# Kernel tuning notes

Hardware: AMD Instinct MI355X
Metric: run time of the kernel (lower is better)

The kernel has to match this reference:

```python
import jax, jax.numpy as jnp
import numpy as np

B, S, E, H = 2, 2048, 1024, 16
HD = E // H
CLAMP = 5.0


def setup_inputs() -> dict:
    key = jax.random.key(0)
    k1, k2, k3, k4 = jax.random.split(key, 4)
    # xavier-uniform-ish scale for weights
    lim_qkv = float(np.sqrt(6.0 / (E + 3 * E)))
    lim_o = float(np.sqrt(6.0 / (E + E)))
    return {
        "x": jax.random.normal(k1, (B, S, E), dtype=jnp.float32),
        "attn_bias": jax.random.normal(k2, (B, H, S, S), dtype=jnp.float32),
        "Wqkv": jax.random.uniform(k3, (3 * E, E), dtype=jnp.float32, minval=-lim_qkv, maxval=lim_qkv),
        "bqkv": jnp.zeros((3 * E,), dtype=jnp.float32),
        "Wo": jax.random.uniform(k4, (E, E), dtype=jnp.float32, minval=-lim_o, maxval=lim_o),
        "bo": jnp.zeros((E,), dtype=jnp.float32),
    }


def reference(x, attn_bias, Wqkv, bqkv, Wo, bo):
    b, s, e = x.shape
    # QKV projection: [B,S,3E] -> [B,S,H,3*HD] -> [B,H,S,3*HD]
    qkv = jnp.einsum("bse,fe->bsf", x, Wqkv) + bqkv
    qkv = qkv.reshape(b, s, H, 3 * HD).transpose(0, 2, 1, 3)
    q, k, v = jnp.split(qkv, 3, axis=-1)  # each [B,H,S,HD]
    # logits: bias added BEFORE 1/sqrt(d_k) scaling (as in source)
    logits = jnp.einsum("bhqd,bhkd->bhqk", q, k)
    logits = (logits + attn_bias) / jnp.sqrt(jnp.float32(HD))
    logits = jnp.clip(logits, -CLAMP, CLAMP)
    attn = jax.nn.softmax(logits, axis=-1)
    vals = jnp.einsum("bhqk,bhkd->bhqd", attn, v)
    vals = vals.transpose(0, 2, 1, 3).reshape(b, s, e)
    return jnp.einsum("bse,fe->bsf", vals, Wo) + bo
```

## Files before the change

### kernel.cpp

```cpp
#include <hip/hip_runtime.h>
#include <hip/hip_bf16.h>

#define NB 2
#define NS 2048
#define NE 1024
#define NH 16
#define HD 64

typedef __hip_bfloat16 bf16;
typedef __attribute__((ext_vector_type(8))) short bf16x8;
typedef __attribute__((ext_vector_type(4))) float f32x4;

typedef __attribute__((address_space(3))) void* lds_p;
typedef const __attribute__((address_space(1))) void* glb_p;

#define MFMA16(a, b, c) __builtin_amdgcn_mfma_f32_16x16x32_bf16((a), (b), (c), 0, 0, 0)

__device__ __forceinline__ void gl_lds16(const void* g, void* l) {
    __builtin_amdgcn_global_load_lds((glb_p)g, (lds_p)l, 16, 0, 0);
}

__device__ __forceinline__ bf16x8 ldv8(const bf16* p) { return *(const bf16x8*)p; }

__global__ __launch_bounds__(256) void cast3_k(const float* __restrict__ x,
                                               const float* __restrict__ wqkv,
                                               const float* __restrict__ wo,
                                               bf16* __restrict__ xb,
                                               bf16* __restrict__ wqkvb,
                                               bf16* __restrict__ wob) {
    const int n_x = NB * NS * NE / 4;
    const int n_q = 3 * NE * NE / 4;
    const int n_o = NE * NE / 4;
    int i = blockIdx.x * 256 + threadIdx.x;
    const float* in;
    bf16* out;
    int j;
    if (i < n_x) {
        in = x; out = xb; j = i;
    } else if (i < n_x + n_q) {
        in = wqkv; out = wqkvb; j = i - n_x;
    } else if (i < n_x + n_q + n_o) {
        in = wo; out = wob; j = i - n_x - n_q;
    } else {
        return;
    }
    float4 v = ((const float4*)in)[j];
    union { ushort4 u; bf16 b[4]; } pk;
    pk.b[0] = __float2bfloat16(v.x);
    pk.b[1] = __float2bfloat16(v.y);
    pk.b[2] = __float2bfloat16(v.z);
    pk.b[3] = __float2bfloat16(v.w);
    ((ushort4*)out)[j] = pk.u;
}

__global__ __launch_bounds__(256) void qkv_gemm(const bf16* __restrict__ A,
                                                const bf16* __restrict__ Bm,
                                                const float* __restrict__ bqkv,
                                                bf16* __restrict__ Qb, bf16* __restrict__ Kb,
                                                bf16* __restrict__ Vtb) {
    __shared__ bf16 As[128 * 32];
    __shared__ bf16 Bs[128 * 32];
    const int brow = blockIdx.x * 128;
    const int bcol = blockIdx.y * 128;
    const int t = threadIdx.x;
    const int w = t >> 6, lane = t & 63;
    const int wr = (w >> 1) * 64, wc = (w & 1) * 64;
    const int lr = lane & 15, lh = lane >> 4;
    const int K = 1024;

    f32x4 acc[4][4];
#pragma unroll
    for (int m = 0; m < 4; ++m)
#pragma unroll
        for (int n = 0; n < 4; ++n) acc[m][n] = (f32x4){0.f, 0.f, 0.f, 0.f};

    const bf16* ga0 = A + (size_t)(brow + (t >> 2)) * K + (t & 3) * 8;
    const bf16* ga1 = A + (size_t)(brow + 64 + (t >> 2)) * K + (t & 3) * 8;
    const bf16* gb0 = Bm + (size_t)(bcol + (t >> 2)) * K + (t & 3) * 8;
    const bf16* gb1 = Bm + (size_t)(bcol + 64 + (t >> 2)) * K + (t & 3) * 8;
    bf16* la0 = As + t * 8;
    bf16* la1 = As + 2048 + t * 8;
    bf16* lb0 = Bs + t * 8;
    bf16* lb1 = Bs + 2048 + t * 8;

    for (int kt = 0; kt < K; kt += 32) {
        gl_lds16(ga0 + kt, la0);
        gl_lds16(ga1 + kt, la1);
        gl_lds16(gb0 + kt, lb0);
        gl_lds16(gb1 + kt, lb1);
        __syncthreads();
        bf16x8 af[4], bfv[4];
#pragma unroll
        for (int m = 0; m < 4; ++m) af[m] = ldv8(&As[(wr + m * 16 + lr) * 32 + lh * 8]);
#pragma unroll
        for (int n = 0; n < 4; ++n) bfv[n] = ldv8(&Bs[(wc + n * 16 + lr) * 32 + lh * 8]);
#pragma unroll
        for (int m = 0; m < 4; ++m)
#pragma unroll
            for (int n = 0; n < 4; ++n) acc[m][n] = MFMA16(af[m], bfv[n], acc[m][n]);
        __syncthreads();
    }

#pragma unroll
    for (int n = 0; n < 4; ++n) {
        const int col = bcol + wc + n * 16 + lr;
        const int h = col / 192;
        const int r = col - h * 192;
        const int wh = r >> 6;
        const int d = r & 63;
        const float bq = bqkv[col];
#pragma unroll
        for (int m = 0; m < 4; ++m) {
            const int row0 = brow + wr + m * 16 + lh * 4;
            const int b = row0 >> 11;
            const int s0 = row0 & 2047;
            const size_t hb = (size_t)(b * NH + h) * (NS * HD);
            if (wh == 2) {
                alignas(8) bf16 tmp[4];
#pragma unroll
                for (int i = 0; i < 4; ++i) tmp[i] = __float2bfloat16(acc[m][n][i] + bq);
                *(ushort4*)(Vtb + hb + (size_t)d * NS + s0) = *(const ushort4*)tmp;
            } else {
                bf16* dst = (wh == 0 ? Qb : Kb) + hb + (size_t)s0 * HD + d;
#pragma unroll
                for (int i = 0; i < 4; ++i) dst[(size_t)i * HD] = __float2bfloat16(acc[m][n][i] + bq);
            }
        }
    }
}

__global__ __launch_bounds__(256, 4) void attn_k(const bf16* __restrict__ Qb,
                                                 const bf16* __restrict__ Kb,
                                                 const bf16* __restrict__ Vtb,
                                                 const float* __restrict__ bias,
                                                 bf16* __restrict__ valsb) {
    const int L = blockIdx.x;
    const int xcd = L & 7, kk = L >> 3;
    const int bh = (xcd << 2) | (kk >> 5);
    const int q0 = (kk & 31) * 64;
    const int t = threadIdx.x;
    const int w = t >> 6, lane = t & 63;
    const int lr = lane & 15, lh = lane >> 4;

    __shared__ bf16 Kls[2][64 * 64];
    __shared__ bf16 Vls[2][64 * 64];
    __shared__ bf16 Ps[4][16 * 64];

    const bf16* Qp = Qb + (size_t)bh * NS * HD;
    const bf16* Kp = Kb + (size_t)bh * NS * HD;
    const bf16* Vp = Vtb + (size_t)bh * HD * NS;

    const int qw = q0 + w * 16;
    bf16x8 qf0 = ldv8(&Qp[(qw + lr) * HD + lh * 8]);
    bf16x8 qf1 = ldv8(&Qp[(qw + lr) * HD + 32 + lh * 8]);

    const float* Bp = bias + (size_t)bh * NS * NS + (size_t)(qw + lr) * NS + lh * 4;

    const int srow0 = t >> 3;
    const int sce0 = ((t & 7) * 8) ^ ((srow0 & 7) << 3);
    const int srow1 = srow0 + 32;
    const int sce1 = ((t & 7) * 8) ^ ((srow1 & 7) << 3);

    f32x4 acc_o[4];
    float rowsum = 0.f;
#pragma unroll
    for (int n = 0; n < 4; ++n) acc_o[n] = (f32x4){0.f, 0.f, 0.f, 0.f};

    const float C1 = 0.18033688011112042f;
    const float C2 = 7.2134752044448170f;

    const int rswz = (lr & 7) << 3;
    const int ce0 = (lh * 8) ^ rswz;
    const int ce1 = (32 + lh * 8) ^ rswz;
    const int pswz = (lr & 7) << 3;

    gl_lds16(Kp + (size_t)srow0 * HD + sce0, &Kls[0][t * 8]);
    gl_lds16(Kp + (size_t)srow1 * HD + sce1, &Kls[0][2048 + t * 8]);
    gl_lds16(Vp + (size_t)srow0 * NS + sce0, &Vls[0][t * 8]);
    gl_lds16(Vp + (size_t)srow1 * NS + sce1, &Vls[0][2048 + t * 8]);
    __builtin_amdgcn_sched_barrier(0);
    float4 bvA[4], bvB[4];
#pragma unroll
    for (int n = 0; n < 4; ++n) bvA[n] = *(const float4*)(Bp + n * 16);
    __builtin_amdgcn_sched_barrier(0);
#pragma unroll
    for (int n = 0; n < 4; ++n) bvB[n] = *(const float4*)(Bp + 64 + n * 16);
    __builtin_amdgcn_sched_barrier(0);
    asm volatile("s_waitcnt vmcnt(8)" ::: "memory");
    __builtin_amdgcn_sched_barrier(0);
    __builtin_amdgcn_s_barrier();
    __builtin_amdgcn_sched_barrier(0);

#define ATTN_COMPUTE(CUR, BV)                                                         \
    {                                                                                 \
        const bf16* Kc = &Kls[CUR][0];                                                \
        f32x4 s[4];                                                                   \
        _Pragma("unroll") for (int n = 0; n < 4; ++n) {                               \
            bf16x8 k0 = ldv8(&Kc[(n * 16 + lr) * 64 + ce0]);                          \
            bf16x8 k1 = ldv8(&Kc[(n * 16 + lr) * 64 + ce1]);                          \
            s[n] = (f32x4){0.f, 0.f, 0.f, 0.f};                                       \
            s[n] = MFMA16(k0, qf0, s[n]);                                             \
            s[n] = MFMA16(k1, qf1, s[n]);                                             \
        }                                                                             \
        _Pragma("unroll") for (int n = 0; n < 4; ++n) {                               \
            union { ushort4 u; bf16 b[4]; } pk;                                       \
            _Pragma("unroll") for (int i = 0; i < 4; ++i) {                           \
                float bb = (i == 0   ? BV[n].x                                        \
                            : i == 1 ? BV[n].y                                        \
                            : i == 2 ? BV[n].z                                        \
                                     : BV[n].w);                                      \
                float xv = (s[n][i] + bb) * C1;                                       \
                xv = fminf(fmaxf(xv, -C2), C2);                                       \
                float p = exp2f(xv);                                                  \
                rowsum += p;                                                          \
                pk.b[i] = __float2bfloat16(p);                                        \
            }                                                                         \
            *(ushort4*)&Ps[w][lr * 64 + ((n * 16 + lh * 4) ^ pswz)] = pk.u;           \
        }                                                                             \
        bf16x8 pa0 = ldv8(&Ps[w][lr * 64 + ((lh * 8) ^ pswz)]);                       \
        bf16x8 pa1 = ldv8(&Ps[w][lr * 64 + (((32 + lh * 8)) ^ pswz)]);                \
        const bf16* Vc = &Vls[CUR][0];                                                \
        _Pragma("unroll") for (int n = 0; n < 4; ++n) {                               \
            bf16x8 v0 = ldv8(&Vc[(n * 16 + lr) * 64 + ce0]);                          \
            bf16x8 v1 = ldv8(&Vc[(n * 16 + lr) * 64 + ce1]);                          \
            acc_o[n] = MFMA16(pa0, v0, acc_o[n]);                                     \
            acc_o[n] = MFMA16(pa1, v1, acc_o[n]);                                     \
        }                                                                             \
    }

#define TILESTEP(CUR, BV, KTN)                                                        \
    {                                                                                 \
        bf16* Kd = &Kls[(CUR) ^ 1][0];                                                \
        bf16* Vd = &Vls[(CUR) ^ 1][0];                                                \
        gl_lds16(Kp + (size_t)((KTN) + srow0) * HD + sce0, Kd + t * 8);               \
        gl_lds16(Kp + (size_t)((KTN) + srow1) * HD + sce1, Kd + 2048 + t * 8);        \
        gl_lds16(Vp + (size_t)srow0 * NS + (KTN) + sce0, Vd + t * 8);                 \
        gl_lds16(Vp + (size_t)srow1 * NS + (KTN) + sce1, Vd + 2048 + t * 8);          \
        __builtin_amdgcn_sched_barrier(0);                                            \
        ATTN_COMPUTE(CUR, BV)                                                         \
        __builtin_amdgcn_sched_barrier(0);                                            \
        _Pragma("unroll") for (int n = 0; n < 4; ++n)                                 \
            BV[n] = *(const float4*)(Bp + (KTN) + 64 + n * 16);                       \
        __builtin_amdgcn_sched_barrier(0);                                            \
        asm volatile("s_waitcnt vmcnt(4)" ::: "memory");                              \
        __builtin_amdgcn_sched_barrier(0);                                            \
        __builtin_amdgcn_s_barrier();                                                 \
        __builtin_amdgcn_sched_barrier(0);                                            \
    }

    for (int it = 0; it < 15; ++it) {
        const int tt = it * 2;
        TILESTEP(0, bvA, (tt + 1) * 64)
        TILESTEP(1, bvB, (tt + 2) * 64)
    }

    {
        const int ktn = 31 * 64;
        bf16* Kd = &Kls[1][0];
        bf16* Vd = &Vls[1][0];
        gl_lds16(Kp + (size_t)(ktn + srow0) * HD + sce0, Kd + t * 8);
        gl_lds16(Kp + (size_t)(ktn + srow1) * HD + sce1, Kd + 2048 + t * 8);
        gl_lds16(Vp + (size_t)srow0 * NS + ktn + sce0, Vd + t * 8);
        gl_lds16(Vp + (size_t)srow1 * NS + ktn + sce1, Vd + 2048 + t * 8);
        __builtin_amdgcn_sched_barrier(0);
        ATTN_COMPUTE(0, bvA)
        __builtin_amdgcn_sched_barrier(0);
        asm volatile("s_waitcnt vmcnt(0)" ::: "memory");
        __builtin_amdgcn_sched_barrier(0);
        __builtin_amdgcn_s_barrier();
        __builtin_amdgcn_sched_barrier(0);
    }
    ATTN_COMPUTE(1, bvB)
#undef TILESTEP
#undef ATTN_COMPUTE

    rowsum += __shfl_xor(rowsum, 16, 64);
    rowsum += __shfl_xor(rowsum, 32, 64);
    float inv[4];
#pragma unroll
    for (int i = 0; i < 4; ++i) inv[i] = 1.0f / __shfl(rowsum, lh * 4 + i, 64);

    const int b = bh >> 4, h = bh & 15;
#pragma unroll
    for (int n = 0; n < 4; ++n) {
#pragma unroll
        for (int i = 0; i < 4; ++i) {
            const int qrow = qw + lh * 4 + i;
            valsb[(size_t)(b * NS + qrow) * NE + h * HD + n * 16 + lr] =
                __float2bfloat16(acc_o[n][i] * inv[i]);
        }
    }
}

__global__ __launch_bounds__(256) void out_gemm(const bf16* __restrict__ A,
                                                const bf16* __restrict__ Bm,
                                                const float* __restrict__ bo,
                                                float* __restrict__ out) {
    __shared__ bf16 As[128 * 32];
    __shared__ bf16 Bs[64 * 32];
    const int brow = blockIdx.x * 128;
    const int bcol = blockIdx.y * 64;
    const int t = threadIdx.x;
    const int w = t >> 6, lane = t & 63;
    const int wr = (w >> 1) * 64, wc = (w & 1) * 32;
    const int lr = lane & 15, lh = lane >> 4;
    const int K = 1024;

    f32x4 acc[4][2];
#pragma unroll
    for (int m = 0; m < 4; ++m)
#pragma unroll
        for (int n = 0; n < 2; ++n) acc[m][n] = (f32x4){0.f, 0.f, 0.f, 0.f};

    const bf16* ga0 = A + (size_t)(brow + (t >> 2)) * K + (t & 3) * 8;
    const bf16* ga1 = A + (size_t)(brow + 64 + (t >> 2)) * K + (t & 3) * 8;
    const bf16* gb0 = Bm + (size_t)(bcol + (t >> 2)) * K + (t & 3) * 8;
    bf16* la0 = As + t * 8;
    bf16* la1 = As + 2048 + t * 8;
    bf16* lb0 = Bs + t * 8;

    for (int kt = 0; kt < K; kt += 32) {
        gl_lds16(ga0 + kt, la0);
        gl_lds16(ga1 + kt, la1);
        gl_lds16(gb0 + kt, lb0);
        __syncthreads();
        bf16x8 af[4], bfv[2];
#pragma unroll
        for (int m = 0; m < 4; ++m) af[m] = ldv8(&As[(wr + m * 16 + lr) * 32 + lh * 8]);
#pragma unroll
        for (int n = 0; n < 2; ++n) bfv[n] = ldv8(&Bs[(wc + n * 16 + lr) * 32 + lh * 8]);
#pragma unroll
        for (int m = 0; m < 4; ++m)
#pragma unroll
            for (int n = 0; n < 2; ++n) acc[m][n] = MFMA16(af[m], bfv[n], acc[m][n]);
        __syncthreads();
    }

#pragma unroll
    for (int n = 0; n < 2; ++n) {
        const int col = bcol + wc + n * 16 + lr;
        const float bv = bo[col];
#pragma unroll
        for (int m = 0; m < 4; ++m) {
            const int row0 = brow + wr + m * 16 + lh * 4;
#pragma unroll
            for (int i = 0; i < 4; ++i) out[(size_t)(row0 + i) * NE + col] = acc[m][n][i] + bv;
        }
    }
}

extern "C" void kernel_launch(void* const* d_in, const int* in_sizes, int n_in,
                              void* d_out, int out_size, void* d_ws, size_t ws_size,
                              hipStream_t stream) {
    const float* x = (const float*)d_in[0];
    const float* attn_bias = (const float*)d_in[1];
    const float* Wqkv = (const float*)d_in[2];
    const float* bqkv = (const float*)d_in[3];
    const float* Wo = (const float*)d_in[4];
    const float* bo = (const float*)d_in[5];
    float* out = (float*)d_out;

    char* ws = (char*)d_ws;
    bf16* xb = (bf16*)(ws);
    bf16* Wqkvb = (bf16*)(ws + (8u << 20));
    bf16* Wob = (bf16*)(ws + (14u << 20));
    bf16* Qb = (bf16*)(ws + (16u << 20));
    bf16* Kb = (bf16*)(ws + (24u << 20));
    bf16* Vtb = (bf16*)(ws + (32u << 20));
    bf16* valsb = (bf16*)(ws + (40u << 20));

    cast3_k<<<8192, 256, 0, stream>>>(x, Wqkv, Wo, xb, Wqkvb, Wob);

    qkv_gemm<<<dim3(32, 24), 256, 0, stream>>>(xb, Wqkvb, bqkv, Qb, Kb, Vtb);

    attn_k<<<dim3(1024), 256, 0, stream>>>(Qb, Kb, Vtb, attn_bias, valsb);

    out_gemm<<<dim3(32, 16), 256, 0, stream>>>(valsb, Wob, bo, out);
}
```

Measured before the change: 212.0 us.

## Load attention bias row-coalesced and transpose through LDS as bf16

Each lane now reads the bias as contiguous float4 chunks along the key dimension, so a wave covers whole 256-byte row segments. The old per-lane MFMA-fragment pattern scattered these reads. The values are converted to bf16 and staged through the per-wave P scratch in LDS, then read back in fragment layout before the score computation. The bias prefetch is moved ahead of the compute, and the stash step is moved after it. This should give better-coalesced global reads of the largest input, at the cost of extra LDS traffic and bf16 rounding of the bias.

```diff
diff --git a/kernel.cpp b/kernel.cpp
--- a/kernel.cpp
+++ b/kernel.cpp
@@ -21,6 +21,12 @@
 }
 
 __device__ __forceinline__ bf16x8 ldv8(const bf16* p) { return *(const bf16x8*)p; }
+
+__device__ __forceinline__ float bf16raw2f(unsigned short v) {
+    union { unsigned u; float f; } c;
+    c.u = ((unsigned)v) << 16;
+    return c.f;
+}
 
 __global__ __launch_bounds__(256) void cast3_k(const float* __restrict__ x,
                                                const float* __restrict__ wqkv,
@@ -154,7 +160,7 @@
     bf16x8 qf0 = ldv8(&Qp[(qw + lr) * HD + lh * 8]);
     bf16x8 qf1 = ldv8(&Qp[(qw + lr) * HD + 32 + lh * 8]);
 
-    const float* Bp = bias + (size_t)bh * NS * NS + (size_t)(qw + lr) * NS + lh * 4;
+    const float* Bst = bias + (size_t)bh * NS * NS + (size_t)(qw + lh) * NS + lr * 4;
 
     const int srow0 = t >> 3;
     const int sce0 = ((t & 7) * 8) ^ ((srow0 & 7) << 3);
@@ -173,28 +179,43 @@
     const int ce0 = (lh * 8) ^ rswz;
     const int ce1 = (32 + lh * 8) ^ rswz;
     const int pswz = (lr & 7) << 3;
+
+    float4 vrA[4], vrB[4];
+
+#define BIAS_STASH(VR)                                                                 \
+    _Pragma("unroll") for (int n = 0; n < 4; ++n) {                                    \
+        union { ushort4 u; bf16 b[4]; } pk;                                            \
+        pk.b[0] = __float2bfloat16(VR[n].x);                                           \
+        pk.b[1] = __float2bfloat16(VR[n].y);                                           \
+        pk.b[2] = __float2bfloat16(VR[n].z);                                           \
+        pk.b[3] = __float2bfloat16(VR[n].w);                                           \
+        const int rr = n * 4 + lh;                                                     \
+        *(ushort4*)&Ps[w][rr * 64 + ((lr * 4) ^ ((rr & 7) << 3))] = pk.u;              \
+    }
 
     gl_lds16(Kp + (size_t)srow0 * HD + sce0, &Kls[0][t * 8]);
     gl_lds16(Kp + (size_t)srow1 * HD + sce1, &Kls[0][2048 + t * 8]);
     gl_lds16(Vp + (size_t)srow0 * NS + sce0, &Vls[0][t * 8]);
     gl_lds16(Vp + (size_t)srow1 * NS + sce1, &Vls[0][2048 + t * 8]);
     __builtin_amdgcn_sched_barrier(0);
-    float4 bvA[4], bvB[4];
-#pragma unroll
-    for (int n = 0; n < 4; ++n) bvA[n] = *(const float4*)(Bp + n * 16);
+#pragma unroll
+    for (int n = 0; n < 4; ++n) vrA[n] = *(const float4*)(Bst + (size_t)(n * 4) * NS);
     __builtin_amdgcn_sched_barrier(0);
 #pragma unroll
-    for (int n = 0; n < 4; ++n) bvB[n] = *(const float4*)(Bp + 64 + n * 16);
+    for (int n = 0; n < 4; ++n) vrB[n] = *(const float4*)(Bst + (size_t)(n * 4) * NS + 64);
     __builtin_amdgcn_sched_barrier(0);
-    asm volatile("s_waitcnt vmcnt(8)" ::: "memory");
+    BIAS_STASH(vrA)
     __builtin_amdgcn_sched_barrier(0);
     __builtin_amdgcn_s_barrier();
     __builtin_amdgcn_sched_barrier(0);
 
-#define ATTN_COMPUTE(CUR, BV)                                                         \
+#define ATTN_COMPUTE(CUR)                                                             \
     {                                                                                 \
         const bf16* Kc = &Kls[CUR][0];                                                \
         f32x4 s[4];                                                                   \
+        ushort4 bu[4];                                                                \
+        _Pragma("unroll") for (int n = 0; n < 4; ++n)                                 \
+            bu[n] = *(const ushort4*)&Ps[w][lr * 64 + ((n * 16 + lh * 4) ^ pswz)];    \
         _Pragma("unroll") for (int n = 0; n < 4; ++n) {                               \
             bf16x8 k0 = ldv8(&Kc[(n * 16 + lr) * 64 + ce0]);                          \
             bf16x8 k1 = ldv8(&Kc[(n * 16 + lr) * 64 + ce1]);                          \
@@ -204,12 +225,10 @@
         }                                                                             \
         _Pragma("unroll") for (int n = 0; n < 4; ++n) {                               \
             union { ushort4 u; bf16 b[4]; } pk;                                       \
+            float bb[4] = {bf16raw2f(bu[n].x), bf16raw2f(bu[n].y),                    \
+                           bf16raw2f(bu[n].z), bf16raw2f(bu[n].w)};                   \
             _Pragma("unroll") for (int i = 0; i < 4; ++i) {                           \
-                float bb = (i == 0   ? BV[n].x                                        \
-                            : i == 1 ? BV[n].y                                        \
-                            : i == 2 ? BV[n].z                                        \
-                                     : BV[n].w);                                      \
-                float xv = (s[n][i] + bb) * C1;                                       \
+                float xv = (s[n][i] + bb[i]) * C1;                                    \
                 xv = fminf(fmaxf(xv, -C2), C2);                                       \
                 float p = exp2f(xv);                                                  \
                 rowsum += p;                                                          \
@@ -228,7 +247,7 @@
         }                                                                             \
     }
 
-#define TILESTEP(CUR, BV, KTN)                                                        \
+#define TILESTEP(CUR, VRC, VRN, KTN)                                                  \
     {                                                                                 \
         bf16* Kd = &Kls[(CUR) ^ 1][0];                                                \
         bf16* Vd = &Vls[(CUR) ^ 1][0];                                                \
@@ -237,10 +256,12 @@
         gl_lds16(Vp + (size_t)srow0 * NS + (KTN) + sce0, Vd + t * 8);                 \
         gl_lds16(Vp + (size_t)srow1 * NS + (KTN) + sce1, Vd + 2048 + t * 8);          \
         __builtin_amdgcn_sched_barrier(0);                                            \
-        ATTN_COMPUTE(CUR, BV)                                                         \
-        __builtin_amdgcn_sched_barrier(0);                                            \
         _Pragma("unroll") for (int n = 0; n < 4; ++n)                                 \
-            BV[n] = *(const float4*)(Bp + (KTN) + 64 + n * 16);                       \
+            VRN[n] = *(const float4*)(Bst + (size_t)(n * 4) * NS + (KTN) + 64);       \
+        __builtin_amdgcn_sched_barrier(0);                                            \
+        ATTN_COMPUTE(CUR)                                                             \
+        __builtin_amdgcn_sched_barrier(0);                                            \
+        BIAS_STASH(VRC)                                                               \
         __builtin_amdgcn_sched_barrier(0);                                            \
         asm volatile("s_waitcnt vmcnt(4)" ::: "memory");                              \
         __builtin_amdgcn_sched_barrier(0);                                            \
@@ -250,8 +271,8 @@
 
     for (int it = 0; it < 15; ++it) {
         const int tt = it * 2;
-        TILESTEP(0, bvA, (tt + 1) * 64)
-        TILESTEP(1, bvB, (tt + 2) * 64)
+        TILESTEP(0, vrB, vrA, (tt + 1) * 64)
+        TILESTEP(1, vrA, vrB, (tt + 2) * 64)
     }
 
     {
@@ -263,16 +284,19 @@
         gl_lds16(Vp + (size_t)srow0 * NS + ktn + sce0, Vd + t * 8);
         gl_lds16(Vp + (size_t)srow1 * NS + ktn + sce1, Vd + 2048 + t * 8);
         __builtin_amdgcn_sched_barrier(0);
-        ATTN_COMPUTE(0, bvA)
+        ATTN_COMPUTE(0)
+        __builtin_amdgcn_sched_barrier(0);
+        BIAS_STASH(vrB)
         __builtin_amdgcn_sched_barrier(0);
         asm volatile("s_waitcnt vmcnt(0)" ::: "memory");
         __builtin_amdgcn_sched_barrier(0);
         __builtin_amdgcn_s_barrier();
         __builtin_amdgcn_sched_barrier(0);
     }
-    ATTN_COMPUTE(1, bvB)
+    ATTN_COMPUTE(1)
 #undef TILESTEP
 #undef ATTN_COMPUTE
+#undef BIAS_STASH
 
     rowsum += __shfl_xor(rowsum, 16, 64);
     rowsum += __shfl_xor(rowsum, 32, 64);
```

New measurement: 216.8 us. +2.3%, slower.
